# Performance work log

Measured on AMD Instinct MI355X. Metric: run time of the kernel, lower is better.

Reference implementation:

```python
import jax, jax.numpy as jnp
import numpy as np

DIM = 1024
HEADS = 16
B, N = 2, 2048


def setup_inputs() -> dict:
    key = jax.random.key(0)
    ks = jax.random.split(key, 10)
    s = 1.0 / np.sqrt(DIM)
    return {
        "y2_for": jax.random.normal(ks[0], (B, N, DIM), jnp.float32),
        "y2_back": jax.random.normal(ks[1], (B, N, DIM), jnp.float32),
        "Wq": jax.random.normal(ks[2], (DIM, DIM), jnp.float32) * s,
        "bq": jnp.zeros((DIM,), jnp.float32),
        "Wk": jax.random.normal(ks[3], (DIM, DIM), jnp.float32) * s,
        "bk": jnp.zeros((DIM,), jnp.float32),
        "Wv": jax.random.normal(ks[4], (DIM, DIM), jnp.float32) * s,
        "bv": jnp.zeros((DIM,), jnp.float32),
        "Wo": jax.random.normal(ks[5], (DIM, DIM), jnp.float32) * s,
        "bo": jnp.zeros((DIM,), jnp.float32),
    }


def reference(y2_for, y2_back, Wq, bq, Wk, bk, Wv, bv, Wo, bo):
    h = HEADS
    d = DIM // h
    scale = d ** -0.5
    q = y2_for @ Wq + bq                    # [b, n, dim]
    k = y2_back @ Wk + bk
    v = (y2_back + y2_for) @ Wv + bv

    def split_heads(x):
        b, n, _ = x.shape
        return x.reshape(b, n, h, d).transpose(0, 2, 1, 3)  # [b, h, n, d]

    q, k, v = split_heads(q), split_heads(k), split_heads(v)
    attn = jax.nn.softmax(jnp.einsum('bhid,bhjd->bhij', q, k) * scale, axis=-1)
    out = jnp.einsum('bhij,bhjd->bhid', attn, v)
    out = out.transpose(0, 2, 1, 3).reshape(y2_for.shape)   # [b, n, dim]
    out = out + y2_for + y2_back
    return out @ Wo + bo
```

## Files before the change

kernel.cpp:

```cpp
#include <hip/hip_runtime.h>

#define DIM 1024
#define HEADS 16
#define BB 2
#define NN 2048
#define HD 64
#define M_ROWS (BB*NN)

typedef __bf16 bf16x8 __attribute__((ext_vector_type(8)));
typedef float f32x4 __attribute__((ext_vector_type(4)));
typedef short s16x4 __attribute__((ext_vector_type(4)));

__device__ inline unsigned short f2bf(float f) {
    unsigned int u = __builtin_bit_cast(unsigned int, f);
    u += 0x7fffu + ((u >> 16) & 1u);
    return (unsigned short)(u >> 16);
}
__device__ inline bf16x8 as_bf16x8(uint4 v) {
    return __builtin_bit_cast(bf16x8, v);
}
__device__ __forceinline__ void gl_lds16(const unsigned short* g, unsigned short* l) {
    __builtin_amdgcn_global_load_lds(
        (const __attribute__((address_space(1))) unsigned int*)g,
        (__attribute__((address_space(3))) unsigned int*)l, 16, 0, 0);
}

__device__ __forceinline__ f32x4 mfma16x16x16bf16(s16x4 a, s16x4 b, f32x4 c) {
#if __has_builtin(__builtin_amdgcn_mfma_f32_16x16x16bf16_1k)
    return __builtin_amdgcn_mfma_f32_16x16x16bf16_1k(a, b, c, 0, 0, 0);
#else
    asm volatile("v_mfma_f32_16x16x16_bf16 %0, %1, %2, %0"
                 : "+v"(c) : "v"(a), "v"(b));
    return c;
#endif
}

__global__ __launch_bounds__(256) void prep_w(
    const float* __restrict__ Wq, const float* __restrict__ Wk,
    const float* __restrict__ Wv, const float* __restrict__ Wo,
    unsigned short* __restrict__ Wt_all)
{
    __shared__ float tile[32][33];
    const int m = blockIdx.z;
    const float* W = (m == 0) ? Wq : (m == 1) ? Wk : (m == 2) ? Wv : Wo;
    const int bk = blockIdx.x, bn = blockIdx.y;
    const int tx = threadIdx.x & 31, ty = threadIdx.x >> 5;

    #pragma unroll
    for (int i = 0; i < 32; i += 8)
        tile[ty + i][tx] = W[(size_t)(bk*32 + ty + i)*DIM + bn*32 + tx];
    __syncthreads();
    unsigned short* dst = Wt_all + (size_t)m * DIM * DIM;
    #pragma unroll
    for (int i = 0; i < 32; i += 8)
        dst[(size_t)(bn*32 + ty + i)*DIM + bk*32 + tx] = f2bf(tile[tx][ty + i]);
}

__global__ __launch_bounds__(256) void prep_act(
    const float* __restrict__ y2f, const float* __restrict__ y2b,
    unsigned short* __restrict__ Af, unsigned short* __restrict__ Ab)
{
    const size_t idx = ((size_t)blockIdx.x*256 + threadIdx.x) * 8;
    float4 f0 = *(const float4*)(y2f + idx);
    float4 f1 = *(const float4*)(y2f + idx + 4);
    float4 b0 = *(const float4*)(y2b + idx);
    float4 b1 = *(const float4*)(y2b + idx + 4);
    ushort4 o0, o1;
    o0.x = f2bf(f0.x); o0.y = f2bf(f0.y); o0.z = f2bf(f0.z); o0.w = f2bf(f0.w);
    o1.x = f2bf(f1.x); o1.y = f2bf(f1.y); o1.z = f2bf(f1.z); o1.w = f2bf(f1.w);
    *(ushort4*)(Af + idx) = o0;
    *(ushort4*)(Af + idx + 4) = o1;
    o0.x = f2bf(b0.x); o0.y = f2bf(b0.y); o0.z = f2bf(b0.z); o0.w = f2bf(b0.w);
    o1.x = f2bf(b1.x); o1.y = f2bf(b1.y); o1.z = f2bf(b1.z); o1.w = f2bf(b1.w);
    *(ushort4*)(Ab + idx) = o0;
    *(ushort4*)(Ab + idx + 4) = o1;
}

__global__ __launch_bounds__(256) void gemm128(
    const unsigned short* __restrict__ Af, const unsigned short* __restrict__ Ab,
    const unsigned short* __restrict__ attp,
    const unsigned short* __restrict__ Wt_all,
    const float* __restrict__ bq, const float* __restrict__ bk,
    const float* __restrict__ bv, const float* __restrict__ bo,
    unsigned short* __restrict__ Qh, unsigned short* __restrict__ Kh,
    unsigned short* __restrict__ Vt, float* __restrict__ out, int mode_base)
{
    const int mode = (mode_base == 3) ? 3
                   : ((blockIdx.z == 0) ? 2 : (int)blockIdx.z - 1);
    __shared__ __align__(16) unsigned short sA[128*32];
    __shared__ __align__(16) unsigned short sB[128*32];
    const int bm = blockIdx.x, bn = blockIdx.y;
    const int t = threadIdx.x;
    const int w = t >> 6, lane = t & 63, ln = lane & 15, quad = lane >> 4;
    const int wm = w >> 1, wn = w & 1;
    const unsigned short* Wt = Wt_all + (size_t)mode * (DIM*DIM);
    const unsigned short* A0 = (mode == 1) ? Ab : (mode == 3) ? attp : Af;

    const int srow = lane >> 2;
    const int scol = (lane & 3) * 8;

    f32x4 acc[4][4];
    #pragma unroll
    for (int mi = 0; mi < 4; mi++)
        #pragma unroll
        for (int ni = 0; ni < 4; ni++)
            acc[mi][ni] = (f32x4){0.f, 0.f, 0.f, 0.f};

    const int niter = (mode == 2) ? 64 : 32;
    for (int it = 0; it < niter; it++) {
        const int kt = it & 31;
        const unsigned short* Asrc = (it >= 32) ? Ab : A0;
        __syncthreads();
        #pragma unroll
        for (int j = 0; j < 2; j++) {
            int row = w*32 + j*16;
            gl_lds16(Asrc + (size_t)(bm*128 + row + srow)*DIM + kt*32 + scol,
                     &sA[row*32]);
            gl_lds16(Wt + (size_t)(bn*128 + row + srow)*DIM + kt*32 + scol,
                     &sB[row*32]);
        }
        __syncthreads();

        bf16x8 af[4], bfr[4];
        #pragma unroll
        for (int mi = 0; mi < 4; mi++)
            af[mi] = as_bf16x8(*(const uint4*)(&sA[(wm*64 + mi*16 + ln)*32 + quad*8]));
        #pragma unroll
        for (int ni = 0; ni < 4; ni++)
            bfr[ni] = as_bf16x8(*(const uint4*)(&sB[(wn*64 + ni*16 + ln)*32 + quad*8]));
        #pragma unroll
        for (int mi = 0; mi < 4; mi++)
            #pragma unroll
            for (int ni = 0; ni < 4; ni++)
                acc[mi][ni] = __builtin_amdgcn_mfma_f32_16x16x32_bf16(af[mi], bfr[ni], acc[mi][ni], 0, 0, 0);
    }

    const float* bias = (mode == 0) ? bq : (mode == 1) ? bk : (mode == 2) ? bv : bo;
    if (mode < 3) {
        unsigned short* dst = (mode == 0) ? Qh : (mode == 1) ? Kh : Vt;
        const float sc = (mode == 0) ? 0.125f * 1.4426950408889634f : 1.0f;
        #pragma unroll
        for (int mi = 0; mi < 4; mi++) {
            #pragma unroll
            for (int r = 0; r < 4; r++) {
                int grow = bm*128 + wm*64 + mi*16 + quad*4 + r;
                int b_ = grow >> 11, n = grow & (NN - 1);
                #pragma unroll
                for (int ni = 0; ni < 4; ni++) {
                    int gcol = bn*128 + wn*64 + ni*16 + ln;
                    int hh = gcol >> 6, dd = gcol & 63;
                    float val = (acc[mi][ni][r] + bias[gcol]) * sc;
                    if (mode == 2)
                        dst[(((size_t)(b_*HEADS + hh))*HD + dd)*NN + n] = f2bf(val);
                    else
                        dst[(((size_t)(b_*HEADS + hh))*NN + n)*HD + dd] = f2bf(val);
                }
            }
        }
    } else {
        #pragma unroll
        for (int mi = 0; mi < 4; mi++) {
            #pragma unroll
            for (int r = 0; r < 4; r++) {
                int grow = bm*128 + wm*64 + mi*16 + quad*4 + r;
                #pragma unroll
                for (int ni = 0; ni < 4; ni++) {
                    int gcol = bn*128 + wn*64 + ni*16 + ln;
                    out[(size_t)grow*DIM + gcol] = acc[mi][ni][r] + bias[gcol];
                }
            }
        }
    }
}

__global__ __launch_bounds__(256) void attn_kernel(
    const unsigned short* __restrict__ Qh, const unsigned short* __restrict__ Kh,
    const unsigned short* __restrict__ Vt, const float* __restrict__ y2f,
    const float* __restrict__ y2b, unsigned short* __restrict__ attp)
{
    const int bh = blockIdx.x;
    const int qt = blockIdx.y;
    const int b = bh >> 4, h = bh & 15;
    const int t = threadIdx.x;
    const int w = t >> 6, lane = t & 63, ln = lane & 15, quad = lane >> 4;
    const int sw = ln & 7;
    const float EBIAS = 17.312340490667562f;

    __shared__ __align__(16) unsigned short sQ[64*64];
    __shared__ __align__(16) unsigned short sK[64*64];
    __shared__ __align__(16) unsigned short sVt[64*64];

    const unsigned short* Qb  = Qh + (size_t)bh * NN * HD + (size_t)qt * 64 * HD;
    const unsigned short* Kb  = Kh + (size_t)bh * NN * HD;
    const unsigned short* Vtb = Vt + (size_t)bh * HD * NN;

    const int rl = lane >> 3, cb = lane & 7;

    #pragma unroll
    for (int j = 0; j < 2; j++) {
        int row = w*16 + j*8 + rl;
        gl_lds16(Qb + (size_t)row*HD + ((cb ^ (row & 7))*8), &sQ[(w*16 + j*8)*64]);
    }

    float lsum = 0.f;
    f32x4 accO[4];
    #pragma unroll
    for (int di = 0; di < 4; di++) accO[di] = (f32x4){0.f, 0.f, 0.f, 0.f};

    for (int jt = 0; jt < 32; jt++) {
        __syncthreads();
        #pragma unroll
        for (int j = 0; j < 2; j++) {
            int row = w*16 + j*8 + rl;
            gl_lds16(Kb + (size_t)(jt*64 + row)*HD + ((cb ^ (row & 7))*8),
                     &sK[(w*16 + j*8)*64]);
            gl_lds16(Vtb + (size_t)row*NN + jt*64 + ((cb ^ (row & 7))*8),
                     &sVt[(w*16 + j*8)*64]);
        }
        __syncthreads();

        f32x4 accS[4];
        #pragma unroll
        for (int ni = 0; ni < 4; ni++) accS[ni] = (f32x4){0.f, 0.f, 0.f, 0.f};
        #pragma unroll
        for (int k0 = 0; k0 < 64; k0 += 32) {
            int blkq = (k0 >> 3) + quad;
            bf16x8 aq = as_bf16x8(*(const uint4*)(&sQ[(w*16 + ln)*64 + ((blkq ^ sw)*8)]));
            #pragma unroll
            for (int ni = 0; ni < 4; ni++) {
                bf16x8 bk = as_bf16x8(*(const uint4*)(&sK[(ni*16 + ln)*64 + ((blkq ^ sw)*8)]));
                accS[ni] = __builtin_amdgcn_mfma_f32_16x16x32_bf16(bk, aq, accS[ni], 0, 0, 0);
            }
        }

        s16x4 pf[4];
        #pragma unroll
        for (int ni = 0; ni < 4; ni++) {
            float e0 = __builtin_amdgcn_exp2f(accS[ni][0] - EBIAS);
            float e1 = __builtin_amdgcn_exp2f(accS[ni][1] - EBIAS);
            float e2 = __builtin_amdgcn_exp2f(accS[ni][2] - EBIAS);
            float e3 = __builtin_amdgcn_exp2f(accS[ni][3] - EBIAS);
            lsum += (e0 + e1) + (e2 + e3);
            unsigned int lo = (__builtin_bit_cast(unsigned int, e1) & 0xFFFF0000u)
                            | (__builtin_bit_cast(unsigned int, e0) >> 16);
            unsigned int hi = (__builtin_bit_cast(unsigned int, e3) & 0xFFFF0000u)
                            | (__builtin_bit_cast(unsigned int, e2) >> 16);
            pf[ni] = __builtin_bit_cast(s16x4, uint2{lo, hi});
        }

        #pragma unroll
        for (int ni = 0; ni < 4; ni++) {
            int blkv = 2*ni + (quad >> 1);
            int off = (quad & 1) * 4;
            #pragma unroll
            for (int di = 0; di < 4; di++) {
                s16x4 bv = __builtin_bit_cast(s16x4,
                    *(const uint2*)(&sVt[(di*16 + ln)*64 + ((blkv ^ sw)*8) + off]));
                accO[di] = mfma16x16x16bf16(pf[ni], bv, accO[di]);
            }
        }
    }

    float L = lsum;
    L += __shfl_xor(L, 16, 64);
    L += __shfl_xor(L, 32, 64);
    #pragma unroll
    for (int r = 0; r < 4; r++) {
        float Lr = __shfl(L, quad*4 + r, 64);
        float inv = 1.f / Lr;
        int n = qt*64 + w*16 + quad*4 + r;
        #pragma unroll
        for (int di = 0; di < 4; di++) {
            int c = h*64 + di*16 + ln;
            size_t gi = ((size_t)b*NN + n)*DIM + c;
            float o = accO[di][r]*inv + y2f[gi] + y2b[gi];
            attp[gi] = f2bf(o);
        }
    }
}

extern "C" void kernel_launch(void* const* d_in, const int* in_sizes, int n_in,
                              void* d_out, int out_size, void* d_ws, size_t ws_size,
                              hipStream_t stream) {
    const float* y2f = (const float*)d_in[0];
    const float* y2b = (const float*)d_in[1];
    const float* Wq  = (const float*)d_in[2];
    const float* bq  = (const float*)d_in[3];
    const float* Wk  = (const float*)d_in[4];
    const float* bk  = (const float*)d_in[5];
    const float* Wv  = (const float*)d_in[6];
    const float* bv  = (const float*)d_in[7];
    const float* Wo  = (const float*)d_in[8];
    const float* bo  = (const float*)d_in[9];
    float* out = (float*)d_out;

    const size_t NACT = (size_t)M_ROWS * DIM;
    unsigned short* ws   = (unsigned short*)d_ws;
    unsigned short* Af   = ws;
    unsigned short* Ab   = ws + NACT;
    unsigned short* Qh   = ws + 2*NACT;
    unsigned short* Kh   = ws + 3*NACT;
    unsigned short* Vt   = ws + 4*NACT;
    unsigned short* Wt   = ws + 5*NACT;
    unsigned short* attp = Ab;

    prep_w<<<dim3(32, 32, 4), 256, 0, stream>>>(Wq, Wk, Wv, Wo, Wt);
    prep_act<<<dim3(2048), 256, 0, stream>>>(y2f, y2b, Af, Ab);
    gemm128<<<dim3(32, 8, 3), 256, 0, stream>>>(
        Af, Ab, attp, Wt, bq, bk, bv, bo, Qh, Kh, Vt, out, 0);
    attn_kernel<<<dim3(32, 32), 256, 0, stream>>>(Qh, Kh, Vt, y2f, y2b, attp);
    gemm128<<<dim3(32, 8, 1), 256, 0, stream>>>(
        Af, Ab, attp, Wt, bq, bk, bv, bo, Qh, Kh, Vt, out, 3);
}
```

Measured before the change: 255.5 us.

## Precompute y2_for+y2_back sum and split QKV/out GEMMs with smaller output tiles

The activation prep kernel now also writes a bf16 copy of y2_for+y2_back, so the V projection runs a single K=1024 pass instead of two passes over Af and Ab. The QKV GEMM is split into its own kernel with a flat grid, giving every block uniform work instead of one slice doing double the iterations. The output projection becomes a separate kernel with 64-row tiles, doubling the block count to 512 for better CU occupancy. The cost is one extra activation write and more workspace. Rounding the sum once in bf16, rather than adding two separately rounded products, slightly changes V numerics.

```diff
diff --git a/kernel.cpp b/kernel.cpp
--- a/kernel.cpp
+++ b/kernel.cpp
@@ -58,43 +58,44 @@
 
 __global__ __launch_bounds__(256) void prep_act(
     const float* __restrict__ y2f, const float* __restrict__ y2b,
-    unsigned short* __restrict__ Af, unsigned short* __restrict__ Ab)
+    unsigned short* __restrict__ Af, unsigned short* __restrict__ Ab,
+    unsigned short* __restrict__ As)
 {
     const size_t idx = ((size_t)blockIdx.x*256 + threadIdx.x) * 8;
-    float4 f0 = *(const float4*)(y2f + idx);
-    float4 f1 = *(const float4*)(y2f + idx + 4);
-    float4 b0 = *(const float4*)(y2b + idx);
-    float4 b1 = *(const float4*)(y2b + idx + 4);
-    ushort4 o0, o1;
-    o0.x = f2bf(f0.x); o0.y = f2bf(f0.y); o0.z = f2bf(f0.z); o0.w = f2bf(f0.w);
-    o1.x = f2bf(f1.x); o1.y = f2bf(f1.y); o1.z = f2bf(f1.z); o1.w = f2bf(f1.w);
-    *(ushort4*)(Af + idx) = o0;
-    *(ushort4*)(Af + idx + 4) = o1;
-    o0.x = f2bf(b0.x); o0.y = f2bf(b0.y); o0.z = f2bf(b0.z); o0.w = f2bf(b0.w);
-    o1.x = f2bf(b1.x); o1.y = f2bf(b1.y); o1.z = f2bf(b1.z); o1.w = f2bf(b1.w);
-    *(ushort4*)(Ab + idx) = o0;
-    *(ushort4*)(Ab + idx + 4) = o1;
-}
-
-__global__ __launch_bounds__(256) void gemm128(
+    #pragma unroll
+    for (int half = 0; half < 2; half++) {
+        float4 f = *(const float4*)(y2f + idx + half*4);
+        float4 b = *(const float4*)(y2b + idx + half*4);
+        ushort4 of, ob, os;
+        of.x = f2bf(f.x); of.y = f2bf(f.y); of.z = f2bf(f.z); of.w = f2bf(f.w);
+        ob.x = f2bf(b.x); ob.y = f2bf(b.y); ob.z = f2bf(b.z); ob.w = f2bf(b.w);
+        os.x = f2bf(f.x + b.x); os.y = f2bf(f.y + b.y);
+        os.z = f2bf(f.z + b.z); os.w = f2bf(f.w + b.w);
+        *(ushort4*)(Af + idx + half*4) = of;
+        *(ushort4*)(Ab + idx + half*4) = ob;
+        *(ushort4*)(As + idx + half*4) = os;
+    }
+}
+
+__global__ __launch_bounds__(256) void gemm_qkv(
     const unsigned short* __restrict__ Af, const unsigned short* __restrict__ Ab,
-    const unsigned short* __restrict__ attp,
+    const unsigned short* __restrict__ As,
     const unsigned short* __restrict__ Wt_all,
     const float* __restrict__ bq, const float* __restrict__ bk,
-    const float* __restrict__ bv, const float* __restrict__ bo,
+    const float* __restrict__ bv,
     unsigned short* __restrict__ Qh, unsigned short* __restrict__ Kh,
-    unsigned short* __restrict__ Vt, float* __restrict__ out, int mode_base)
-{
-    const int mode = (mode_base == 3) ? 3
-                   : ((blockIdx.z == 0) ? 2 : (int)blockIdx.z - 1);
+    unsigned short* __restrict__ Vt)
+{
+    const int bm = blockIdx.x;
+    const int mode = blockIdx.y >> 3;
+    const int bn = blockIdx.y & 7;
     __shared__ __align__(16) unsigned short sA[128*32];
     __shared__ __align__(16) unsigned short sB[128*32];
-    const int bm = blockIdx.x, bn = blockIdx.y;
     const int t = threadIdx.x;
     const int w = t >> 6, lane = t & 63, ln = lane & 15, quad = lane >> 4;
     const int wm = w >> 1, wn = w & 1;
     const unsigned short* Wt = Wt_all + (size_t)mode * (DIM*DIM);
-    const unsigned short* A0 = (mode == 1) ? Ab : (mode == 3) ? attp : Af;
+    const unsigned short* A0 = (mode == 0) ? Af : (mode == 1) ? Ab : As;
 
     const int srow = lane >> 2;
     const int scol = (lane & 3) * 8;
@@ -106,15 +107,12 @@
         for (int ni = 0; ni < 4; ni++)
             acc[mi][ni] = (f32x4){0.f, 0.f, 0.f, 0.f};
 
-    const int niter = (mode == 2) ? 64 : 32;
-    for (int it = 0; it < niter; it++) {
-        const int kt = it & 31;
-        const unsigned short* Asrc = (it >= 32) ? Ab : A0;
+    for (int kt = 0; kt < 32; kt++) {
         __syncthreads();
         #pragma unroll
         for (int j = 0; j < 2; j++) {
             int row = w*32 + j*16;
-            gl_lds16(Asrc + (size_t)(bm*128 + row + srow)*DIM + kt*32 + scol,
+            gl_lds16(A0 + (size_t)(bm*128 + row + srow)*DIM + kt*32 + scol,
                      &sA[row*32]);
             gl_lds16(Wt + (size_t)(bn*128 + row + srow)*DIM + kt*32 + scol,
                      &sB[row*32]);
@@ -135,39 +133,87 @@
                 acc[mi][ni] = __builtin_amdgcn_mfma_f32_16x16x32_bf16(af[mi], bfr[ni], acc[mi][ni], 0, 0, 0);
     }
 
-    const float* bias = (mode == 0) ? bq : (mode == 1) ? bk : (mode == 2) ? bv : bo;
-    if (mode < 3) {
-        unsigned short* dst = (mode == 0) ? Qh : (mode == 1) ? Kh : Vt;
-        const float sc = (mode == 0) ? 0.125f * 1.4426950408889634f : 1.0f;
-        #pragma unroll
-        for (int mi = 0; mi < 4; mi++) {
-            #pragma unroll
-            for (int r = 0; r < 4; r++) {
-                int grow = bm*128 + wm*64 + mi*16 + quad*4 + r;
-                int b_ = grow >> 11, n = grow & (NN - 1);
-                #pragma unroll
-                for (int ni = 0; ni < 4; ni++) {
-                    int gcol = bn*128 + wn*64 + ni*16 + ln;
-                    int hh = gcol >> 6, dd = gcol & 63;
-                    float val = (acc[mi][ni][r] + bias[gcol]) * sc;
-                    if (mode == 2)
-                        dst[(((size_t)(b_*HEADS + hh))*HD + dd)*NN + n] = f2bf(val);
-                    else
-                        dst[(((size_t)(b_*HEADS + hh))*NN + n)*HD + dd] = f2bf(val);
-                }
+    const float* bias = (mode == 0) ? bq : (mode == 1) ? bk : bv;
+    unsigned short* dst = (mode == 0) ? Qh : (mode == 1) ? Kh : Vt;
+    const float sc = (mode == 0) ? 0.125f * 1.4426950408889634f : 1.0f;
+    #pragma unroll
+    for (int mi = 0; mi < 4; mi++) {
+        #pragma unroll
+        for (int r = 0; r < 4; r++) {
+            int grow = bm*128 + wm*64 + mi*16 + quad*4 + r;
+            int b_ = grow >> 11, n = grow & (NN - 1);
+            #pragma unroll
+            for (int ni = 0; ni < 4; ni++) {
+                int gcol = bn*128 + wn*64 + ni*16 + ln;
+                int hh = gcol >> 6, dd = gcol & 63;
+                float val = (acc[mi][ni][r] + bias[gcol]) * sc;
+                if (mode == 2)
+                    dst[(((size_t)(b_*HEADS + hh))*HD + dd)*NN + n] = f2bf(val);
+                else
+                    dst[(((size_t)(b_*HEADS + hh))*NN + n)*HD + dd] = f2bf(val);
             }
         }
-    } else {
-        #pragma unroll
-        for (int mi = 0; mi < 4; mi++) {
-            #pragma unroll
-            for (int r = 0; r < 4; r++) {
-                int grow = bm*128 + wm*64 + mi*16 + quad*4 + r;
-                #pragma unroll
-                for (int ni = 0; ni < 4; ni++) {
-                    int gcol = bn*128 + wn*64 + ni*16 + ln;
-                    out[(size_t)grow*DIM + gcol] = acc[mi][ni][r] + bias[gcol];
-                }
+    }
+}
+
+__global__ __launch_bounds__(256) void gemm_out(
+    const unsigned short* __restrict__ attp,
+    const unsigned short* __restrict__ Wt_all,
+    const float* __restrict__ bo, float* __restrict__ out)
+{
+    const int bm = blockIdx.x, bn = blockIdx.y;
+    __shared__ __align__(16) unsigned short sA[64*32];
+    __shared__ __align__(16) unsigned short sB[128*32];
+    const int t = threadIdx.x;
+    const int w = t >> 6, lane = t & 63, ln = lane & 15, quad = lane >> 4;
+    const int wm = w >> 1, wn = w & 1;
+    const unsigned short* Wt = Wt_all + (size_t)3 * (DIM*DIM);
+
+    const int srow = lane >> 2;
+    const int scol = (lane & 3) * 8;
+
+    f32x4 acc[2][4];
+    #pragma unroll
+    for (int mi = 0; mi < 2; mi++)
+        #pragma unroll
+        for (int ni = 0; ni < 4; ni++)
+            acc[mi][ni] = (f32x4){0.f, 0.f, 0.f, 0.f};
+
+    for (int kt = 0; kt < 32; kt++) {
+        __syncthreads();
+        gl_lds16(attp + (size_t)(bm*64 + w*16 + srow)*DIM + kt*32 + scol,
+                 &sA[(w*16)*32]);
+        #pragma unroll
+        for (int j = 0; j < 2; j++) {
+            int row = w*32 + j*16;
+            gl_lds16(Wt + (size_t)(bn*128 + row + srow)*DIM + kt*32 + scol,
+                     &sB[row*32]);
+        }
+        __syncthreads();
+
+        bf16x8 af[2], bfr[4];
+        #pragma unroll
+        for (int mi = 0; mi < 2; mi++)
+            af[mi] = as_bf16x8(*(const uint4*)(&sA[(wm*32 + mi*16 + ln)*32 + quad*8]));
+        #pragma unroll
+        for (int ni = 0; ni < 4; ni++)
+            bfr[ni] = as_bf16x8(*(const uint4*)(&sB[(wn*64 + ni*16 + ln)*32 + quad*8]));
+        #pragma unroll
+        for (int mi = 0; mi < 2; mi++)
+            #pragma unroll
+            for (int ni = 0; ni < 4; ni++)
+                acc[mi][ni] = __builtin_amdgcn_mfma_f32_16x16x32_bf16(af[mi], bfr[ni], acc[mi][ni], 0, 0, 0);
+    }
+
+    #pragma unroll
+    for (int mi = 0; mi < 2; mi++) {
+        #pragma unroll
+        for (int r = 0; r < 4; r++) {
+            int grow = bm*64 + wm*32 + mi*16 + quad*4 + r;
+            #pragma unroll
+            for (int ni = 0; ni < 4; ni++) {
+                int gcol = bn*128 + wn*64 + ni*16 + ln;
+                out[(size_t)grow*DIM + gcol] = acc[mi][ni][r] + bo[gcol];
             }
         }
     }
@@ -298,17 +344,17 @@
     unsigned short* ws   = (unsigned short*)d_ws;
     unsigned short* Af   = ws;
     unsigned short* Ab   = ws + NACT;
-    unsigned short* Qh   = ws + 2*NACT;
-    unsigned short* Kh   = ws + 3*NACT;
-    unsigned short* Vt   = ws + 4*NACT;
-    unsigned short* Wt   = ws + 5*NACT;
+    unsigned short* As   = ws + 2*NACT;
+    unsigned short* Qh   = ws + 3*NACT;
+    unsigned short* Kh   = ws + 4*NACT;
+    unsigned short* Vt   = ws + 5*NACT;
+    unsigned short* Wt   = ws + 6*NACT;
     unsigned short* attp = Ab;
 
     prep_w<<<dim3(32, 32, 4), 256, 0, stream>>>(Wq, Wk, Wv, Wo, Wt);
-    prep_act<<<dim3(2048), 256, 0, stream>>>(y2f, y2b, Af, Ab);
-    gemm128<<<dim3(32, 8, 3), 256, 0, stream>>>(
-        Af, Ab, attp, Wt, bq, bk, bv, bo, Qh, Kh, Vt, out, 0);
+    prep_act<<<dim3(2048), 256, 0, stream>>>(y2f, y2b, Af, Ab, As);
+    gemm_qkv<<<dim3(32, 24), 256, 0, stream>>>(
+        Af, Ab, As, Wt, bq, bk, bv, Qh, Kh, Vt);
     attn_kernel<<<dim3(32, 32), 256, 0, stream>>>(Qh, Kh, Vt, y2f, y2b, attp);
-    gemm128<<<dim3(32, 8, 1), 256, 0, stream>>>(
-        Af, Ab, attp, Wt, bq, bk, bv, bo, Qh, Kh, Vt, out, 3);
-}
+    gemm_out<<<dim3(64, 8), 256, 0, stream>>>(attp, Wt, bo, out);
+}
```

Result: faster. 226.8 us (-11.2%).
